# Kernel tuning notes

Measured on AMD Instinct MI355X. Metric: run time of the kernel, lower is better.

Reference implementation:

```python
import jax, jax.numpy as jnp
import numpy as np

TEMP = 1.0

def setup_inputs() -> dict:
    key = jax.random.key(0)
    k1, k2 = jax.random.split(key)
    B, T, C, Vp1 = 16, 2048, 256, 1025
    z = jax.random.normal(k1, (B, T, C), dtype=jnp.float32)
    mask = jnp.ones((B, T, 1), dtype=jnp.float32)
    codebook_weight = jax.random.normal(k2, (Vp1, C), dtype=jnp.float32)
    return {"z": z, "mask": mask, "codebook_weight": codebook_weight}

def reference(z, mask, codebook_weight):
    # e = codebook.embedding.weight.clone().detach()[1:, :]
    e = jax.lax.stop_gradient(codebook_weight[1:, :])  # [V, C]
    b, t, c = z.shape
    V = e.shape[0]
    z_flat = z.reshape(-1, c)                          # [N, C], N = b*t
    # sim(): cosine-sim matmul + log_softmax + argmax one-hot quantize
    cos_sim = jnp.matmul(z_flat, e.T)                  # [N, V]
    log_probs = jax.nn.log_softmax(cos_sim / TEMP, axis=1)
    indices = jnp.argmax(log_probs, axis=1)            # [N]
    # one_hot @ e is exactly a row gather -- avoid materializing one_hot
    z_q = e[indices]                                   # [N, C]
    z_q3 = z_q.reshape(b, t, c)
    # loss(): masked commitment + smoothness
    valid_count = mask.sum() * c
    commitment_loss = (jnp.square(z - jax.lax.stop_gradient(z_q3)) * mask).sum() / valid_count
    smoothness_loss = (jnp.square(z[:, :-1, :] - z[:, 1:, :]) * mask[:, 1:, :]).sum() / valid_count
    # codebook_usage(): (one_hot * mask).sum(0) / mask.sum(), normalized
    mflat = mask.reshape(-1)                           # [N]
    prob = jax.ops.segment_sum(mflat, indices, num_segments=V) / mflat.sum()
    e_mean = prob / prob.sum()
    return (smoothness_loss, commitment_loss, log_probs.reshape(b, t, V), z_q3, e_mean)
```

## Files before the change

kernel.cpp:

```cpp
#include <hip/hip_runtime.h>
#include <hip/hip_bf16.h>

#define TPB 512
#define BM 32
#define NROW 32768
#define NBLK (NROW / BM)
#define VV 1024
#define KD 256
#define TT 2048

#define LP_OFF 2L
#define ZQ_OFF (2L + 33554432L)
#define EM_OFF (33554434L + 8388608L)

#define WS_HIST 0
#define WS_CSUM 1024
#define WS_SSUM 2048
#define WS_MSUM 3072
#define WS_E8 4096
#define WS_Z8G (4096 + 131072)
#define WS_NEED_Z ((size_t)WS_Z8G * 4 + (size_t)NROW * KD * 2)

typedef __attribute__((ext_vector_type(8))) short bf16x8;
typedef __attribute__((ext_vector_type(4))) float f32x4;

__device__ __forceinline__ void gl_lds16(const void* g, void* l) {
  __builtin_amdgcn_global_load_lds(
      (const __attribute__((address_space(1))) void*)g,
      (__attribute__((address_space(3))) void*)l, 16, 0, 0);
}

__device__ __forceinline__ unsigned short f2bf(float x) {
  unsigned u = __float_as_uint(x);
  unsigned r = ((u >> 16) & 1u) + 0x7FFFu;
  return (unsigned short)((u + r) >> 16);
}

__device__ __forceinline__ unsigned foldf(float v) {
  unsigned b = __float_as_uint(v);
  return b ^ ((unsigned)((int)b >> 31) | 0x80000000u);
}
__device__ __forceinline__ float unfoldf(unsigned k) {
  unsigned s = (unsigned)((int)k >> 31);
  return __uint_as_float(k ^ (0x80000000u | (~s & 0x7FFFFFFFu)));
}

__device__ __forceinline__ int4 pack8(const float* p) {
  float4 a = *(const float4*)p;
  float4 b = *(const float4*)(p + 4);
  int4 pk;
  pk.x = f2bf(a.x) | ((unsigned)f2bf(a.y) << 16);
  pk.y = f2bf(a.z) | ((unsigned)f2bf(a.w) << 16);
  pk.z = f2bf(b.x) | ((unsigned)f2bf(b.y) << 16);
  pk.w = f2bf(b.z) | ((unsigned)f2bf(b.w) << 16);
  return pk;
}

__global__ __launch_bounds__(256) void tok_prep(
    const float* __restrict__ z, const float* __restrict__ cw,
    unsigned short* __restrict__ e8, unsigned short* __restrict__ z8g) {
  int t = blockIdx.x * 256 + threadIdx.x;
  if (t < 1048576) {
    int blk = t >> 10, oct = (t >> 5) & 31, row = t & 31;
    *(int4*)(z8g + ((size_t)t << 3)) =
        pack8(z + ((size_t)((blk << 5) + row) << 8) + (oct << 3));
    return;
  }
  int t2 = t - 1048576;
  if (t2 >= 32768) return;
  int s = t2 >> 12, w = (t2 >> 9) & 7, g = (t2 >> 7) & 3, c = t2 & 127;
  int n = (w << 7) + c;
  int o = (s << 2) + g;
  *(int4*)(e8 + ((size_t)t2 << 3)) =
      pack8(cw + ((size_t)(1 + n) << 8) + (o << 3));
}

__global__ __launch_bounds__(TPB, 4) void tok_mfma(
    const float* __restrict__ z, const float* __restrict__ mask,
    const float* __restrict__ cw, const unsigned short* __restrict__ e8,
    const unsigned short* __restrict__ z8g, float* __restrict__ out,
    float* __restrict__ ws) {
  __shared__ __align__(16) unsigned short Bs[32768];
  __shared__ __align__(16) unsigned char apool[4736];
  unsigned(*wkey)[2][33] = (unsigned(*)[2][33])apool;
  float(*wsum)[33] = (float(*)[33])(apool + 2112);
  float* lse_s = (float*)(apool + 3168);
  float(*exv_s)[4] = (float(*)[4])(apool + 3296);
  int(*exi_s)[4] = (int(*)[4])(apool + 3808);
  int* argi = (int*)(apool + 4320);
  float* cred = (float*)(apool + 4448);
  float* sred = (float*)(apool + 4480);

  const int tid = threadIdx.x;
  const int lane = tid & 63;
  const int w = tid >> 6;
  const int g = lane >> 4;
  const int lm = lane & 15;
  const int c0 = w << 7;
  const int n0 = blockIdx.x * BM;

  const bf16x8* Az = (const bf16x8*)z8g + ((size_t)blockIdx.x << 10);

#pragma unroll
  for (int r = 0; r < 8; ++r)
    gl_lds16(e8 + (((w << 9) + (r << 6) + lane) << 3),
             &Bs[(((w << 9) + (r << 6)) + lane) << 3]);

  f32x4 accA[8], accB[8];
  const f32x4 zzero = {0.f, 0.f, 0.f, 0.f};
#pragma unroll
  for (int nt = 0; nt < 8; ++nt) { accA[nt] = zzero; accB[nt] = zzero; }

  bf16x8 a0 = Az[(g << 5) + lm];
  bf16x8 a1 = Az[(g << 5) + 16 + lm];
  const bf16x8* Bl = (const bf16x8*)&Bs[((w << 9) + (g << 7) + lm) << 3];

#pragma unroll 1
  for (int s = 0; s < 8; ++s) {
    asm volatile("s_waitcnt vmcnt(0)" ::: "memory");
    bf16x8 na0, na1;
    if (s < 7) {
      na0 = Az[((((s + 1) << 2) + g) << 5) + lm];
      na1 = Az[((((s + 1) << 2) + g) << 5) + 16 + lm];
    }
#pragma unroll
    for (int nt = 0; nt < 8; ++nt) {
      bf16x8 b = Bl[nt << 4];
      accA[nt] = __builtin_amdgcn_mfma_f32_16x16x32_bf16(a0, b, accA[nt], 0, 0, 0);
      accB[nt] = __builtin_amdgcn_mfma_f32_16x16x32_bf16(a1, b, accB[nt], 0, 0, 0);
    }
    asm volatile("s_waitcnt lgkmcnt(0)" ::: "memory");
    if (s < 7) {
#pragma unroll
      for (int r = 0; r < 8; ++r)
        gl_lds16(e8 + ((((s + 1) << 12) + (w << 9) + (r << 6) + lane) << 3),
                 &Bs[(((w << 9) + (r << 6)) + lane) << 3]);
    }
    a0 = na0;
    a1 = na1;
  }

  unsigned colpack[8];
#pragma unroll
  for (int nt = 0; nt < 8; ++nt)
    colpack[nt] = 1023u - (unsigned)(c0 + (nt << 4) + lm);

  auto phase1 = [&](f32x4(&ac)[8], int mt) {
#pragma unroll
    for (int j = 0; j < 4; ++j) {
      const int r = (mt << 4) + (g << 2) + j;
      unsigned cur[8];
#pragma unroll
      for (int nt = 0; nt < 8; ++nt)
        cur[nt] = (foldf(ac[nt][j]) & 0xFFFFFC00u) | colpack[nt];
      unsigned k1 = cur[0];
#pragma unroll
      for (int nt = 1; nt < 8; ++nt) k1 = k1 > cur[nt] ? k1 : cur[nt];
#pragma unroll
      for (int d = 1; d <= 8; d <<= 1) {
        unsigned o2 = __shfl_xor(k1, d);
        k1 = k1 > o2 ? k1 : o2;
      }
      const float mw = unfoldf(k1 & 0xFFFFFC00u);
      float sum = 0.f;
#pragma unroll
      for (int nt = 0; nt < 8; ++nt) sum += __expf(ac[nt][j] - mw);
#pragma unroll
      for (int d = 1; d <= 8; d <<= 1) sum += __shfl_xor(sum, d);
#pragma unroll
      for (int nt = 0; nt < 8; ++nt)
        if (cur[nt] == k1) cur[nt] = 0u;
      unsigned k2 = cur[0];
#pragma unroll
      for (int nt = 1; nt < 8; ++nt) k2 = k2 > cur[nt] ? k2 : cur[nt];
#pragma unroll
      for (int d = 1; d <= 8; d <<= 1) {
        unsigned o2 = __shfl_xor(k2, d);
        k2 = k2 > o2 ? k2 : o2;
      }
      if (lm == 0) {
        wkey[w][0][r] = k1;
        wkey[w][1][r] = k2;
        wsum[w][r] = sum;
      }
    }
  };
  phase1(accA, 0);
  phase1(accB, 1);
  __syncthreads();

  if (tid < 32) {
    const int r = tid;
    unsigned best[4] = {0u, 0u, 0u, 0u};
#pragma unroll
    for (int w2 = 0; w2 < 8; ++w2)
#pragma unroll
      for (int k = 0; k < 2; ++k) {
        unsigned x = wkey[w2][k][r];
#pragma unroll
        for (int q = 0; q < 4; ++q) {
          unsigned mx = x > best[q] ? x : best[q];
          unsigned mn = x > best[q] ? best[q] : x;
          best[q] = mx;
          x = mn;
        }
      }
    const float M = unfoldf(best[0] & 0xFFFFFC00u);
    float S = 0.f;
#pragma unroll
    for (int w2 = 0; w2 < 8; ++w2)
      S += wsum[w2][r] * __expf(unfoldf(wkey[w2][0][r] & 0xFFFFFC00u) - M);
    lse_s[r] = M + __logf(S);
#pragma unroll
    for (int q = 0; q < 4; ++q) exi_s[r][q] = (int)(1023u - (best[q] & 0x3FFu));
  }
  __syncthreads();

  {
    const int row = (w << 2) + (lane >> 4);
    const int cd = (lane >> 2) & 3;
    const int seg = lane & 3;
    const int cand = exi_s[row][cd];
    const float* er = cw + (size_t)(1 + cand) * KD + (seg << 6);
    const float* zr = z + (size_t)(n0 + row) * KD + (seg << 6);
    float s = 0.f;
#pragma unroll
    for (int i2 = 0; i2 < 16; ++i2) {
      float4 a4 = *(const float4*)(zr + (i2 << 2));
      float4 b4 = *(const float4*)(er + (i2 << 2));
      s += a4.x * b4.x + a4.y * b4.y + a4.z * b4.z + a4.w * b4.w;
    }
    s += __shfl_xor(s, 1);
    s += __shfl_xor(s, 2);
    if (seg == 0) exv_s[row][cd] = s;
  }
  __syncthreads();

  if (tid < 32) {
    const int row = tid;
    float bv = exv_s[row][0];
    int bi = exi_s[row][0];
#pragma unroll
    for (int c = 1; c < 4; ++c) {
      float v = exv_s[row][c];
      int ci = exi_s[row][c];
      if (v > bv || (v == bv && ci < bi)) { bv = v; bi = ci; }
    }
    argi[row] = bi;
    atomicAdd(&ws[WS_HIST + bi], mask[n0 + row]);
  }
  __syncthreads();

  float csum = 0.f, ssum = 0.f;
  float4 evs[4];
  const bool has_prev = (n0 % TT) != 0;
#pragma unroll
  for (int i = 0; i < 4; ++i) {
    const int r = (i << 3) + w;
    const int c4 = lane << 2;
    const int idx = argi[r];
    const float4 ev = *(const float4*)&cw[(size_t)(1 + idx) * KD + c4];
    evs[i] = ev;
    const float4 zv = *(const float4*)&z[(size_t)(n0 + r) * KD + c4];
    const float mk = mask[n0 + r];
    float dx = zv.x - ev.x, dy = zv.y - ev.y, dz2 = zv.z - ev.z,
          dw = zv.w - ev.w;
    csum += mk * (dx * dx + dy * dy + dz2 * dz2 + dw * dw);
    if (r > 0 || has_prev) {
      const float4 pv = *(const float4*)&z[(size_t)(n0 + r - 1) * KD + c4];
      float ax = zv.x - pv.x, ay = zv.y - pv.y, az = zv.z - pv.z,
            aw = zv.w - pv.w;
      ssum += mk * (ax * ax + ay * ay + az * az + aw * aw);
    }
  }
#pragma unroll
  for (int d = 1; d <= 32; d <<= 1) {
    csum += __shfl_xor(csum, d);
    ssum += __shfl_xor(ssum, d);
  }
  if (lane == 0) { cred[w] = csum; sred[w] = ssum; }
  __syncthreads();
  if (tid == 0) {
    float cs = 0.f, ss2 = 0.f;
#pragma unroll
    for (int i = 0; i < 8; ++i) { cs += cred[i]; ss2 += sred[i]; }
    ws[WS_CSUM + blockIdx.x] = cs;
    ws[WS_SSUM + blockIdx.x] = ss2;
    float ms = 0.f;
    for (int r2 = 0; r2 < BM; ++r2) ms += mask[n0 + r2];
    ws[WS_MSUM + blockIdx.x] = ms;
  }

#pragma unroll
  for (int i = 0; i < 4; ++i) {
    const int r = (i << 3) + w;
    *(float4*)&out[ZQ_OFF + (size_t)(n0 + r) * KD + (lane << 2)] = evs[i];
  }
  auto phase3 = [&](f32x4(&ac)[8], int mt) {
#pragma unroll
    for (int j = 0; j < 4; ++j) {
      const int r = (mt << 4) + (g << 2) + j;
      const float lse = lse_s[r];
      size_t base = LP_OFF + (size_t)(n0 + r) * VV;
#pragma unroll
      for (int nt = 0; nt < 8; ++nt)
        out[base + c0 + (nt << 4) + lm] = ac[nt][j] - lse;
    }
  };
  phase3(accA, 0);
  phase3(accB, 1);
}

__global__ __launch_bounds__(256, 2) void tok_fb(
    const float* __restrict__ z, const float* __restrict__ mask,
    const float* __restrict__ cw, float* __restrict__ out,
    float* __restrict__ ws) {
  __shared__ __align__(16) float z_s[BM][KD];
  __shared__ int argi_s[BM];
  __shared__ float cred[4], sred[4];
  const int tid = threadIdx.x;
  const int lane = tid & 63;
  const int wave = tid >> 6;
  const int n0 = blockIdx.x * BM;
  const float* e = cw + KD;
#pragma unroll
  for (int i = 0; i < 8; ++i) {
    int seg = wave * 8 + i;
    gl_lds16(&z[(size_t)(n0 + seg) * KD + lane * 4], &z_s[seg][0]);
  }
  __syncthreads();
  float acc[8][16];
#pragma unroll
  for (int r = 0; r < 8; ++r)
#pragma unroll
    for (int m = 0; m < 16; ++m) acc[r][m] = 0.f;
#pragma unroll 1
  for (int i = 0; i < 64; ++i) {
    float4 ef[16];
#pragma unroll
    for (int m = 0; m < 16; ++m)
      ef[m] = *(const float4*)&e[(size_t)((m << 6) + lane) * KD + (i << 2)];
    float4 zf[8];
#pragma unroll
    for (int rr = 0; rr < 8; ++rr)
      zf[rr] = *(const float4*)&z_s[(wave << 3) + rr][i << 2];
#pragma unroll
    for (int m = 0; m < 16; ++m)
#pragma unroll
      for (int rr = 0; rr < 8; ++rr)
        acc[rr][m] += zf[rr].x * ef[m].x + zf[rr].y * ef[m].y +
                      zf[rr].z * ef[m].z + zf[rr].w * ef[m].w;
  }
  const int rowbase = wave << 3;
#pragma unroll
  for (int rr = 0; rr < 8; ++rr) {
    float mv = acc[rr][0];
    int mc = lane;
#pragma unroll
    for (int m = 1; m < 16; ++m) {
      float v = acc[rr][m];
      int c = (m << 6) + lane;
      bool tk = v > mv;
      mc = tk ? c : mc;
      mv = tk ? v : mv;
    }
#pragma unroll
    for (int d = 32; d >= 1; d >>= 1) {
      float ov = __shfl_xor(mv, d);
      int oc = __shfl_xor(mc, d);
      bool tk = (ov > mv) || (ov == mv && oc < mc);
      mv = tk ? ov : mv;
      mc = tk ? oc : mc;
    }
    float sum = 0.f;
#pragma unroll
    for (int m = 0; m < 16; ++m) sum += __expf(acc[rr][m] - mv);
#pragma unroll
    for (int d = 32; d >= 1; d >>= 1) sum += __shfl_xor(sum, d);
    float lse = mv + __logf(sum);
    size_t base = LP_OFF + (size_t)(n0 + rowbase + rr) * VV;
#pragma unroll
    for (int m = 0; m < 16; ++m) out[base + (m << 6) + lane] = acc[rr][m] - lse;
    if (lane == 0) {
      argi_s[rowbase + rr] = mc;
      atomicAdd(&ws[WS_HIST + mc], mask[n0 + rowbase + rr]);
    }
  }
  __syncthreads();
  float csum = 0.f, ssum = 0.f;
  const bool has_prev = (n0 % TT) != 0;
#pragma unroll
  for (int i = 0; i < 8; ++i) {
    int q = i * 256 + tid;
    int r = q >> 6;
    int c4 = (q & 63) << 2;
    int idx = argi_s[r];
    const float4 ev = *(const float4*)&e[(size_t)idx * KD + c4];
    const float4 zv = *(const float4*)&z_s[r][c4];
    *(float4*)&out[ZQ_OFF + (size_t)(n0 + r) * KD + c4] = ev;
    float mk = mask[n0 + r];
    float dx = zv.x - ev.x, dy = zv.y - ev.y, dz2 = zv.z - ev.z, dw = zv.w - ev.w;
    csum += mk * (dx * dx + dy * dy + dz2 * dz2 + dw * dw);
    if (r > 0) {
      const float4 pv = *(const float4*)&z_s[r - 1][c4];
      float ax = zv.x - pv.x, ay = zv.y - pv.y, az = zv.z - pv.z, aw = zv.w - pv.w;
      ssum += mk * (ax * ax + ay * ay + az * az + aw * aw);
    } else if (has_prev) {
      const float4 pv = *(const float4*)&z[(size_t)(n0 - 1) * KD + c4];
      float ax = zv.x - pv.x, ay = zv.y - pv.y, az = zv.z - pv.z, aw = zv.w - pv.w;
      ssum += mk * (ax * ax + ay * ay + az * az + aw * aw);
    }
  }
#pragma unroll
  for (int d = 32; d >= 1; d >>= 1) {
    csum += __shfl_xor(csum, d);
    ssum += __shfl_xor(ssum, d);
  }
  if (lane == 0) { cred[wave] = csum; sred[wave] = ssum; }
  __syncthreads();
  if (tid == 0) {
    ws[WS_CSUM + blockIdx.x] = cred[0] + cred[1] + cred[2] + cred[3];
    ws[WS_SSUM + blockIdx.x] = sred[0] + sred[1] + sred[2] + sred[3];
    float ms = 0.f;
    for (int r2 = 0; r2 < BM; ++r2) ms += mask[n0 + r2];
    ws[WS_MSUM + blockIdx.x] = ms;
  }
}

__global__ __launch_bounds__(1024) void tok_final(const float* __restrict__ ws,
                                                  float* __restrict__ out) {
  const int t = threadIdx.x;
  const int lane = t & 63, w = t >> 6;
  __shared__ float red[16];
  auto blockReduce = [&](float v) -> float {
#pragma unroll
    for (int d = 32; d >= 1; d >>= 1) v += __shfl_xor(v, d);
    __syncthreads();
    if (lane == 0) red[w] = v;
    __syncthreads();
    float s = 0.f;
#pragma unroll
    for (int i = 0; i < 16; ++i) s += red[i];
    return s;
  };
  float Mtot = blockReduce(ws[WS_MSUM + t]);
  float Ctot = blockReduce(ws[WS_CSUM + t]);
  float Stot = blockReduce(ws[WS_SSUM + t]);
  float prob = ws[WS_HIST + t] / Mtot;
  float psum = blockReduce(prob);
  out[EM_OFF + t] = prob / psum;
  if (t == 0) {
    float vc = Mtot * (float)KD;
    out[0] = Stot / vc;
    out[1] = Ctot / vc;
  }
}

extern "C" void kernel_launch(void* const* d_in, const int* in_sizes, int n_in,
                              void* d_out, int out_size, void* d_ws,
                              size_t ws_size, hipStream_t stream) {
  const float* z = (const float*)d_in[0];
  const float* mask = (const float*)d_in[1];
  const float* cw = (const float*)d_in[2];
  float* out = (float*)d_out;
  float* ws = (float*)d_ws;
  hipMemsetAsync(ws, 0, 1024 * sizeof(float), stream);
  if (ws_size >= WS_NEED_Z) {
    unsigned short* e8 = (unsigned short*)(ws + WS_E8);
    unsigned short* z8g = (unsigned short*)(ws + WS_Z8G);
    tok_prep<<<4224, 256, 0, stream>>>(z, cw, e8, z8g);
    tok_mfma<<<NBLK, TPB, 0, stream>>>(z, mask, cw, e8, z8g, out, ws);
  } else {
    tok_fb<<<NBLK, 256, 0, stream>>>(z, mask, cw, out, ws);
  }
  tok_final<<<1, 1024, 0, stream>>>(ws, out);
}
```

Baseline: 117.8 us.

## Enlarge row tile to 64 with 16 waves and double-buffered codebook staging

Each block now covers 64 rows with 1024 threads (16 waves), so every wave owns 64 codebook columns. Z tiles are staged into LDS instead of being read per wave from global memory. Codebook slices are loaded as two half-buffers so the global-to-LDS copy of one half overlaps MFMA work on the other. This halves the block count and per-row B traffic, and mask reads now go through LDS. In exchange it uses more LDS per block and more threads per block, which may limit occupancy.

```diff
diff --git a/kernel.cpp b/kernel.cpp
--- a/kernel.cpp
+++ b/kernel.cpp
@@ -1,10 +1,9 @@
 #include <hip/hip_runtime.h>
 #include <hip/hip_bf16.h>
 
-#define TPB 512
-#define BM 32
+#define BM 64
 #define NROW 32768
-#define NBLK (NROW / BM)
+#define NB2 (NROW / BM)
 #define VV 1024
 #define KD 256
 #define TT 2048
@@ -61,101 +60,125 @@
     unsigned short* __restrict__ e8, unsigned short* __restrict__ z8g) {
   int t = blockIdx.x * 256 + threadIdx.x;
   if (t < 1048576) {
-    int blk = t >> 10, oct = (t >> 5) & 31, row = t & 31;
+    int blk = t >> 11, oct = (t >> 6) & 31, row = t & 63;
     *(int4*)(z8g + ((size_t)t << 3)) =
-        pack8(z + ((size_t)((blk << 5) + row) << 8) + (oct << 3));
+        pack8(z + (size_t)((blk << 6) + row) * KD + (oct << 3));
     return;
   }
   int t2 = t - 1048576;
   if (t2 >= 32768) return;
-  int s = t2 >> 12, w = (t2 >> 9) & 7, g = (t2 >> 7) & 3, c = t2 & 127;
-  int n = (w << 7) + c;
-  int o = (s << 2) + g;
-  *(int4*)(e8 + ((size_t)t2 << 3)) =
-      pack8(cw + ((size_t)(1 + n) << 8) + (o << 3));
-}
-
-__global__ __launch_bounds__(TPB, 4) void tok_mfma(
+  int s = t2 >> 12, w2 = (t2 >> 8) & 15, h = (t2 >> 7) & 1,
+      qq = (t2 >> 6) & 1, gp = (t2 >> 5) & 1, c = t2 & 31;
+  int n = (w2 << 6) + (h << 5) + c;
+  int o = (s << 2) + (qq << 1) + gp;
+  *(int4*)(e8 + ((size_t)t2 << 3)) = pack8(cw + (size_t)(1 + n) * KD + (o << 3));
+}
+
+__global__ __launch_bounds__(1024, 4) void tok_mfma(
     const float* __restrict__ z, const float* __restrict__ mask,
     const float* __restrict__ cw, const unsigned short* __restrict__ e8,
     const unsigned short* __restrict__ z8g, float* __restrict__ out,
     float* __restrict__ ws) {
-  __shared__ __align__(16) unsigned short Bs[32768];
-  __shared__ __align__(16) unsigned char apool[4736];
-  unsigned(*wkey)[2][33] = (unsigned(*)[2][33])apool;
-  float(*wsum)[33] = (float(*)[33])(apool + 2112);
-  float* lse_s = (float*)(apool + 3168);
-  float(*exv_s)[4] = (float(*)[4])(apool + 3296);
-  int(*exi_s)[4] = (int(*)[4])(apool + 3808);
-  int* argi = (int*)(apool + 4320);
-  float* cred = (float*)(apool + 4448);
-  float* sred = (float*)(apool + 4480);
+  __shared__ __align__(16) unsigned short A_s[16640];
+  __shared__ __align__(16) unsigned short B_s[32768];
+  __shared__ unsigned wkey[16][2][65];
+  __shared__ float wsum[16][65];
+  __shared__ float lse_s[64];
+  __shared__ float exv_s[64][4];
+  __shared__ int exi_s[64][4];
+  __shared__ int argi[64];
+  __shared__ float mask_s[64];
+  __shared__ float cred[16], sred[16];
 
   const int tid = threadIdx.x;
   const int lane = tid & 63;
   const int w = tid >> 6;
   const int g = lane >> 4;
   const int lm = lane & 15;
-  const int c0 = w << 7;
-  const int n0 = blockIdx.x * BM;
-
-  const bf16x8* Az = (const bf16x8*)z8g + ((size_t)blockIdx.x << 10);
-
-#pragma unroll
-  for (int r = 0; r < 8; ++r)
-    gl_lds16(e8 + (((w << 9) + (r << 6) + lane) << 3),
-             &Bs[(((w << 9) + (r << 6)) + lane) << 3]);
-
-  f32x4 accA[8], accB[8];
+  const int q = g >> 1, g2 = g & 1;
+  const int n0 = blockIdx.x << 6;
+
+  unsigned short* Bw = B_s + (w << 11);
+
+  {
+    const unsigned short* asrc =
+        z8g + ((((size_t)blockIdx.x << 11) + (w << 7)) << 3) + (lane << 3);
+    gl_lds16(asrc, A_s + (w << 1) * 520);
+    gl_lds16(asrc + 512, A_s + ((w << 1) + 1) * 520);
+  }
+  if (tid < 64) mask_s[tid] = mask[n0 + tid];
+  __syncthreads();
+
+  auto stage_half = [&](int s2, int h2, int bufb) {
+    const unsigned short* src =
+        e8 + ((size_t)((((s2 << 4) + w) << 2) + (h2 << 1)) << 9) + (lane << 3);
+    unsigned short* dst = Bw + (bufb << 10);
+    gl_lds16(src, dst);
+    gl_lds16(src + 512, dst + 512);
+  };
+  stage_half(0, 0, 0);
+  stage_half(0, 1, 1);
+
+  f32x4 acc[4][4];
   const f32x4 zzero = {0.f, 0.f, 0.f, 0.f};
 #pragma unroll
-  for (int nt = 0; nt < 8; ++nt) { accA[nt] = zzero; accB[nt] = zzero; }
-
-  bf16x8 a0 = Az[(g << 5) + lm];
-  bf16x8 a1 = Az[(g << 5) + 16 + lm];
-  const bf16x8* Bl = (const bf16x8*)&Bs[((w << 9) + (g << 7) + lm) << 3];
+  for (int mt = 0; mt < 4; ++mt)
+#pragma unroll
+    for (int nt = 0; nt < 4; ++nt) acc[mt][nt] = zzero;
+
+  const int boff = (q << 9) + (g2 << 8) + (lm << 3);
 
 #pragma unroll 1
   for (int s = 0; s < 8; ++s) {
-    asm volatile("s_waitcnt vmcnt(0)" ::: "memory");
-    bf16x8 na0, na1;
-    if (s < 7) {
-      na0 = Az[((((s + 1) << 2) + g) << 5) + lm];
-      na1 = Az[((((s + 1) << 2) + g) << 5) + 16 + lm];
-    }
-#pragma unroll
-    for (int nt = 0; nt < 8; ++nt) {
-      bf16x8 b = Bl[nt << 4];
-      accA[nt] = __builtin_amdgcn_mfma_f32_16x16x32_bf16(a0, b, accA[nt], 0, 0, 0);
-      accB[nt] = __builtin_amdgcn_mfma_f32_16x16x32_bf16(a1, b, accB[nt], 0, 0, 0);
+    asm volatile("s_waitcnt vmcnt(2)" ::: "memory");
+    bf16x8 a[4];
+#pragma unroll
+    for (int mt = 0; mt < 4; ++mt)
+      a[mt] = *(const bf16x8*)(A_s + ((s << 2) + g) * 520 +
+                               (((mt << 4) + lm) << 3));
+#pragma unroll
+    for (int l = 0; l < 2; ++l) {
+      bf16x8 b = *(const bf16x8*)(Bw + boff + (l << 7));
+#pragma unroll
+      for (int mt = 0; mt < 4; ++mt)
+        acc[mt][l] =
+            __builtin_amdgcn_mfma_f32_16x16x32_bf16(a[mt], b, acc[mt][l], 0, 0, 0);
     }
     asm volatile("s_waitcnt lgkmcnt(0)" ::: "memory");
-    if (s < 7) {
-#pragma unroll
-      for (int r = 0; r < 8; ++r)
-        gl_lds16(e8 + ((((s + 1) << 12) + (w << 9) + (r << 6) + lane) << 3),
-                 &Bs[(((w << 9) + (r << 6)) + lane) << 3]);
-    }
-    a0 = na0;
-    a1 = na1;
-  }
-
-  unsigned colpack[8];
-#pragma unroll
-  for (int nt = 0; nt < 8; ++nt)
-    colpack[nt] = 1023u - (unsigned)(c0 + (nt << 4) + lm);
-
-  auto phase1 = [&](f32x4(&ac)[8], int mt) {
+    if (s < 7) stage_half(s + 1, 0, 0);
+    if (s < 7)
+      asm volatile("s_waitcnt vmcnt(2)" ::: "memory");
+    else
+      asm volatile("s_waitcnt vmcnt(0)" ::: "memory");
+#pragma unroll
+    for (int l = 0; l < 2; ++l) {
+      bf16x8 b = *(const bf16x8*)(Bw + 1024 + boff + (l << 7));
+#pragma unroll
+      for (int mt = 0; mt < 4; ++mt)
+        acc[mt][2 + l] = __builtin_amdgcn_mfma_f32_16x16x32_bf16(
+            a[mt], b, acc[mt][2 + l], 0, 0, 0);
+    }
+    asm volatile("s_waitcnt lgkmcnt(0)" ::: "memory");
+    if (s < 7) stage_half(s + 1, 1, 1);
+  }
+
+  unsigned colpack[4];
+#pragma unroll
+  for (int nt = 0; nt < 4; ++nt)
+    colpack[nt] = 1023u - (unsigned)((w << 6) + (nt << 4) + lm);
+
+#pragma unroll
+  for (int mt = 0; mt < 4; ++mt)
 #pragma unroll
     for (int j = 0; j < 4; ++j) {
       const int r = (mt << 4) + (g << 2) + j;
-      unsigned cur[8];
-#pragma unroll
-      for (int nt = 0; nt < 8; ++nt)
-        cur[nt] = (foldf(ac[nt][j]) & 0xFFFFFC00u) | colpack[nt];
+      unsigned cur[4];
+#pragma unroll
+      for (int nt = 0; nt < 4; ++nt)
+        cur[nt] = (foldf(acc[mt][nt][j]) & 0xFFFFFC00u) | colpack[nt];
       unsigned k1 = cur[0];
 #pragma unroll
-      for (int nt = 1; nt < 8; ++nt) k1 = k1 > cur[nt] ? k1 : cur[nt];
+      for (int nt = 1; nt < 4; ++nt) k1 = k1 > cur[nt] ? k1 : cur[nt];
 #pragma unroll
       for (int d = 1; d <= 8; d <<= 1) {
         unsigned o2 = __shfl_xor(k1, d);
@@ -164,15 +187,15 @@
       const float mw = unfoldf(k1 & 0xFFFFFC00u);
       float sum = 0.f;
 #pragma unroll
-      for (int nt = 0; nt < 8; ++nt) sum += __expf(ac[nt][j] - mw);
+      for (int nt = 0; nt < 4; ++nt) sum += __expf(acc[mt][nt][j] - mw);
 #pragma unroll
       for (int d = 1; d <= 8; d <<= 1) sum += __shfl_xor(sum, d);
 #pragma unroll
-      for (int nt = 0; nt < 8; ++nt)
+      for (int nt = 0; nt < 4; ++nt)
         if (cur[nt] == k1) cur[nt] = 0u;
       unsigned k2 = cur[0];
 #pragma unroll
-      for (int nt = 1; nt < 8; ++nt) k2 = k2 > cur[nt] ? k2 : cur[nt];
+      for (int nt = 1; nt < 4; ++nt) k2 = k2 > cur[nt] ? k2 : cur[nt];
 #pragma unroll
       for (int d = 1; d <= 8; d <<= 1) {
         unsigned o2 = __shfl_xor(k2, d);
@@ -184,42 +207,40 @@
         wsum[w][r] = sum;
       }
     }
-  };
-  phase1(accA, 0);
-  phase1(accB, 1);
-  __syncthreads();
-
-  if (tid < 32) {
+  __syncthreads();
+
+  if (tid < 64) {
     const int r = tid;
     unsigned best[4] = {0u, 0u, 0u, 0u};
 #pragma unroll
-    for (int w2 = 0; w2 < 8; ++w2)
+    for (int w2 = 0; w2 < 16; ++w2)
 #pragma unroll
       for (int k = 0; k < 2; ++k) {
         unsigned x = wkey[w2][k][r];
 #pragma unroll
-        for (int q = 0; q < 4; ++q) {
-          unsigned mx = x > best[q] ? x : best[q];
-          unsigned mn = x > best[q] ? best[q] : x;
-          best[q] = mx;
+        for (int p2 = 0; p2 < 4; ++p2) {
+          unsigned mx = x > best[p2] ? x : best[p2];
+          unsigned mn = x > best[p2] ? best[p2] : x;
+          best[p2] = mx;
           x = mn;
         }
       }
     const float M = unfoldf(best[0] & 0xFFFFFC00u);
     float S = 0.f;
 #pragma unroll
-    for (int w2 = 0; w2 < 8; ++w2)
+    for (int w2 = 0; w2 < 16; ++w2)
       S += wsum[w2][r] * __expf(unfoldf(wkey[w2][0][r] & 0xFFFFFC00u) - M);
     lse_s[r] = M + __logf(S);
 #pragma unroll
-    for (int q = 0; q < 4; ++q) exi_s[r][q] = (int)(1023u - (best[q] & 0x3FFu));
+    for (int p2 = 0; p2 < 4; ++p2)
+      exi_s[r][p2] = (int)(1023u - (best[p2] & 0x3FFu));
   }
   __syncthreads();
 
   {
-    const int row = (w << 2) + (lane >> 4);
-    const int cd = (lane >> 2) & 3;
-    const int seg = lane & 3;
+    const int row = tid >> 4;
+    const int cd = (tid >> 2) & 3;
+    const int seg = tid & 3;
     const int cand = exi_s[row][cd];
     const float* er = cw + (size_t)(1 + cand) * KD + (seg << 6);
     const float* zr = z + (size_t)(n0 + row) * KD + (seg << 6);
@@ -236,7 +257,7 @@
   }
   __syncthreads();
 
-  if (tid < 32) {
+  if (tid < 64) {
     const int row = tid;
     float bv = exv_s[row][0];
     int bi = exi_s[row][0];
@@ -247,7 +268,7 @@
       if (v > bv || (v == bv && ci < bi)) { bv = v; bi = ci; }
     }
     argi[row] = bi;
-    atomicAdd(&ws[WS_HIST + bi], mask[n0 + row]);
+    atomicAdd(&ws[WS_HIST + bi], mask_s[row]);
   }
   __syncthreads();
 
@@ -256,13 +277,13 @@
   const bool has_prev = (n0 % TT) != 0;
 #pragma unroll
   for (int i = 0; i < 4; ++i) {
-    const int r = (i << 3) + w;
+    const int r = (i << 4) + w;
     const int c4 = lane << 2;
     const int idx = argi[r];
     const float4 ev = *(const float4*)&cw[(size_t)(1 + idx) * KD + c4];
     evs[i] = ev;
     const float4 zv = *(const float4*)&z[(size_t)(n0 + r) * KD + c4];
-    const float mk = mask[n0 + r];
+    const float mk = mask_s[r];
     float dx = zv.x - ev.x, dy = zv.y - ev.y, dz2 = zv.z - ev.z,
           dw = zv.w - ev.w;
     csum += mk * (dx * dx + dy * dy + dz2 * dz2 + dw * dw);
@@ -283,45 +304,43 @@
   if (tid == 0) {
     float cs = 0.f, ss2 = 0.f;
 #pragma unroll
-    for (int i = 0; i < 8; ++i) { cs += cred[i]; ss2 += sred[i]; }
+    for (int i = 0; i < 16; ++i) { cs += cred[i]; ss2 += sred[i]; }
     ws[WS_CSUM + blockIdx.x] = cs;
     ws[WS_SSUM + blockIdx.x] = ss2;
     float ms = 0.f;
-    for (int r2 = 0; r2 < BM; ++r2) ms += mask[n0 + r2];
+    for (int r2 = 0; r2 < 64; ++r2) ms += mask_s[r2];
     ws[WS_MSUM + blockIdx.x] = ms;
   }
 
 #pragma unroll
   for (int i = 0; i < 4; ++i) {
-    const int r = (i << 3) + w;
+    const int r = (i << 4) + w;
     *(float4*)&out[ZQ_OFF + (size_t)(n0 + r) * KD + (lane << 2)] = evs[i];
   }
-  auto phase3 = [&](f32x4(&ac)[8], int mt) {
+#pragma unroll
+  for (int mt = 0; mt < 4; ++mt)
 #pragma unroll
     for (int j = 0; j < 4; ++j) {
       const int r = (mt << 4) + (g << 2) + j;
       const float lse = lse_s[r];
-      size_t base = LP_OFF + (size_t)(n0 + r) * VV;
-#pragma unroll
-      for (int nt = 0; nt < 8; ++nt)
-        out[base + c0 + (nt << 4) + lm] = ac[nt][j] - lse;
-    }
-  };
-  phase3(accA, 0);
-  phase3(accB, 1);
+      size_t base = LP_OFF + (size_t)(n0 + r) * VV + (w << 6);
+#pragma unroll
+      for (int nt = 0; nt < 4; ++nt)
+        out[base + (nt << 4) + lm] = acc[mt][nt][j] - lse;
+    }
 }
 
 __global__ __launch_bounds__(256, 2) void tok_fb(
     const float* __restrict__ z, const float* __restrict__ mask,
     const float* __restrict__ cw, float* __restrict__ out,
     float* __restrict__ ws) {
-  __shared__ __align__(16) float z_s[BM][KD];
-  __shared__ int argi_s[BM];
+  __shared__ __align__(16) float z_s[32][KD];
+  __shared__ int argi_s[32];
   __shared__ float cred[4], sred[4];
   const int tid = threadIdx.x;
   const int lane = tid & 63;
   const int wave = tid >> 6;
-  const int n0 = blockIdx.x * BM;
+  const int n0 = blockIdx.x * 32;
   const float* e = cw + KD;
 #pragma unroll
   for (int i = 0; i < 8; ++i) {
@@ -422,11 +441,12 @@
     ws[WS_CSUM + blockIdx.x] = cred[0] + cred[1] + cred[2] + cred[3];
     ws[WS_SSUM + blockIdx.x] = sred[0] + sred[1] + sred[2] + sred[3];
     float ms = 0.f;
-    for (int r2 = 0; r2 < BM; ++r2) ms += mask[n0 + r2];
+    for (int r2 = 0; r2 < 32; ++r2) ms += mask[n0 + r2];
     ws[WS_MSUM + blockIdx.x] = ms;
   }
 }
 
+template <int NB>
 __global__ __launch_bounds__(1024) void tok_final(const float* __restrict__ ws,
                                                   float* __restrict__ out) {
   const int t = threadIdx.x;
@@ -443,9 +463,9 @@
     for (int i = 0; i < 16; ++i) s += red[i];
     return s;
   };
-  float Mtot = blockReduce(ws[WS_MSUM + t]);
-  float Ctot = blockReduce(ws[WS_CSUM + t]);
-  float Stot = blockReduce(ws[WS_SSUM + t]);
+  float Mtot = blockReduce(t < NB ? ws[WS_MSUM + t] : 0.f);
+  float Ctot = blockReduce(t < NB ? ws[WS_CSUM + t] : 0.f);
+  float Stot = blockReduce(t < NB ? ws[WS_SSUM + t] : 0.f);
   float prob = ws[WS_HIST + t] / Mtot;
   float psum = blockReduce(prob);
   out[EM_OFF + t] = prob / psum;
@@ -469,9 +489,10 @@
     unsigned short* e8 = (unsigned short*)(ws + WS_E8);
     unsigned short* z8g = (unsigned short*)(ws + WS_Z8G);
     tok_prep<<<4224, 256, 0, stream>>>(z, cw, e8, z8g);
-    tok_mfma<<<NBLK, TPB, 0, stream>>>(z, mask, cw, e8, z8g, out, ws);
+    tok_mfma<<<NB2, 1024, 0, stream>>>(z, mask, cw, e8, z8g, out, ws);
+    tok_final<NB2><<<1, 1024, 0, stream>>>(ws, out);
   } else {
-    tok_fb<<<NBLK, 256, 0, stream>>>(z, mask, cw, out, ws);
-  }
-  tok_final<<<1, 1024, 0, stream>>>(ws, out);
-}
+    tok_fb<<<NROW / 32, 256, 0, stream>>>(z, mask, cw, out, ws);
+    tok_final<NROW / 32><<<1, 1024, 0, stream>>>(ws, out);
+  }
+}
```

Measured after the change: 123.0 us. +4.4%, slower.

## Convert z to bf16 in-kernel via swizzled LDS and stream codebook from global

Applied to the files above, without the earlier changes.

Drops the prep pass that converted all of z to bf16 in workspace. Each block now packs its own 32 rows of z into a swizzled LDS tile, and codebook fragments are read directly from global (L2) into registers with a double-buffered software pipeline instead of being staged through a 64KB LDS buffer. The LDS footprint shrinks, which may raise occupancy. Logits and z_q outputs are written with nontemporal stores to limit cache pollution. The risk is that B fragments read from global may stall the MFMAs more than the LDS path did.

```diff
diff --git a/kernel.cpp b/kernel.cpp
--- a/kernel.cpp
+++ b/kernel.cpp
@@ -18,8 +18,7 @@
 #define WS_SSUM 2048
 #define WS_MSUM 3072
 #define WS_E8 4096
-#define WS_Z8G (4096 + 131072)
-#define WS_NEED_Z ((size_t)WS_Z8G * 4 + (size_t)NROW * KD * 2)
+#define WS_NEED ((size_t)(4096 + 131072) * 4)
 
 typedef __attribute__((ext_vector_type(8))) short bf16x8;
 typedef __attribute__((ext_vector_type(4))) float f32x4;
@@ -56,40 +55,28 @@
   return pk;
 }
 
-__global__ __launch_bounds__(256) void tok_prep(
-    const float* __restrict__ z, const float* __restrict__ cw,
-    unsigned short* __restrict__ e8, unsigned short* __restrict__ z8g) {
+__global__ __launch_bounds__(256) void tok_prep(const float* __restrict__ cw,
+                                                unsigned short* __restrict__ e8) {
   int t = blockIdx.x * 256 + threadIdx.x;
-  if (t < 1048576) {
-    int blk = t >> 10, oct = (t >> 5) & 31, row = t & 31;
-    *(int4*)(z8g + ((size_t)t << 3)) =
-        pack8(z + ((size_t)((blk << 5) + row) << 8) + (oct << 3));
-    return;
-  }
-  int t2 = t - 1048576;
-  if (t2 >= 32768) return;
-  int s = t2 >> 12, w = (t2 >> 9) & 7, g = (t2 >> 7) & 3, c = t2 & 127;
+  int s = t >> 12, w = (t >> 9) & 7, g = (t >> 7) & 3, c = t & 127;
   int n = (w << 7) + c;
   int o = (s << 2) + g;
-  *(int4*)(e8 + ((size_t)t2 << 3)) =
-      pack8(cw + ((size_t)(1 + n) << 8) + (o << 3));
+  *(int4*)(e8 + ((size_t)t << 3)) = pack8(cw + (size_t)(1 + n) * KD + (o << 3));
 }
 
 __global__ __launch_bounds__(TPB, 4) void tok_mfma(
     const float* __restrict__ z, const float* __restrict__ mask,
     const float* __restrict__ cw, const unsigned short* __restrict__ e8,
-    const unsigned short* __restrict__ z8g, float* __restrict__ out,
-    float* __restrict__ ws) {
-  __shared__ __align__(16) unsigned short Bs[32768];
-  __shared__ __align__(16) unsigned char apool[4736];
-  unsigned(*wkey)[2][33] = (unsigned(*)[2][33])apool;
-  float(*wsum)[33] = (float(*)[33])(apool + 2112);
-  float* lse_s = (float*)(apool + 3168);
-  float(*exv_s)[4] = (float(*)[4])(apool + 3296);
-  int(*exi_s)[4] = (int(*)[4])(apool + 3808);
-  int* argi = (int*)(apool + 4320);
-  float* cred = (float*)(apool + 4448);
-  float* sred = (float*)(apool + 4480);
+    float* __restrict__ out, float* __restrict__ ws) {
+  __shared__ __align__(16) unsigned char smem[16384];
+  unsigned(*wkey)[2][33] = (unsigned(*)[2][33])smem;
+  float(*wsum)[33] = (float(*)[33])(smem + 2112);
+  float* lse_s = (float*)(smem + 3168);
+  float(*exv_s)[4] = (float(*)[4])(smem + 3296);
+  int(*exi_s)[4] = (int(*)[4])(smem + 3808);
+  int* argi = (int*)(smem + 4320);
+  float* cred = (float*)(smem + 4448);
+  float* sred = (float*)(smem + 4480);
 
   const int tid = threadIdx.x;
   const int lane = tid & 63;
@@ -99,46 +86,62 @@
   const int c0 = w << 7;
   const int n0 = blockIdx.x * BM;
 
-  const bf16x8* Az = (const bf16x8*)z8g + ((size_t)blockIdx.x << 10);
-
-#pragma unroll
-  for (int r = 0; r < 8; ++r)
-    gl_lds16(e8 + (((w << 9) + (r << 6) + lane) << 3),
-             &Bs[(((w << 9) + (r << 6)) + lane) << 3]);
-
+  {
+    const int zr = (w << 2) + (lane >> 4);
+    const int oc0 = lm << 1;
+    const float* zp = z + (size_t)(n0 + zr) * KD + (lm << 4);
+    int4 p0 = pack8(zp);
+    int4 p1 = pack8(zp + 8);
+    const int i0 = (oc0 << 5) + (zr ^ ((oc0 & 7) << 2));
+    const int i1 = ((oc0 + 1) << 5) + (zr ^ (((oc0 + 1) & 7) << 2));
+    *(int4*)&smem[i0 << 4] = p0;
+    *(int4*)&smem[i1 << 4] = p1;
+  }
+  __syncthreads();
+
+  const bf16x8* Bp = (const bf16x8*)e8 + ((w << 9) + (g << 7) + lm);
   f32x4 accA[8], accB[8];
   const f32x4 zzero = {0.f, 0.f, 0.f, 0.f};
 #pragma unroll
   for (int nt = 0; nt < 8; ++nt) { accA[nt] = zzero; accB[nt] = zzero; }
 
-  bf16x8 a0 = Az[(g << 5) + lm];
-  bf16x8 a1 = Az[(g << 5) + 16 + lm];
-  const bf16x8* Bl = (const bf16x8*)&Bs[((w << 9) + (g << 7) + lm) << 3];
-
-#pragma unroll 1
-  for (int s = 0; s < 8; ++s) {
-    asm volatile("s_waitcnt vmcnt(0)" ::: "memory");
-    bf16x8 na0, na1;
-    if (s < 7) {
-      na0 = Az[((((s + 1) << 2) + g) << 5) + lm];
-      na1 = Az[((((s + 1) << 2) + g) << 5) + 16 + lm];
-    }
-#pragma unroll
-    for (int nt = 0; nt < 8; ++nt) {
-      bf16x8 b = Bl[nt << 4];
-      accA[nt] = __builtin_amdgcn_mfma_f32_16x16x32_bf16(a0, b, accA[nt], 0, 0, 0);
-      accB[nt] = __builtin_amdgcn_mfma_f32_16x16x32_bf16(a1, b, accB[nt], 0, 0, 0);
-    }
-    asm volatile("s_waitcnt lgkmcnt(0)" ::: "memory");
-    if (s < 7) {
-#pragma unroll
-      for (int r = 0; r < 8; ++r)
-        gl_lds16(e8 + ((((s + 1) << 12) + (w << 9) + (r << 6) + lane) << 3),
-                 &Bs[(((w << 9) + (r << 6)) + lane) << 3]);
-    }
-    a0 = na0;
-    a1 = na1;
-  }
+  bf16x8 q0, q1, q2, q3, q4, q5, q6, q7;
+  bf16x8 r0, r1, r2, r3, r4, r5, r6, r7;
+#define LOAD8(P, T)                                                      \
+  P##0 = Bp[((T) << 12)];        P##1 = Bp[((T) << 12) + 16];            \
+  P##2 = Bp[((T) << 12) + 32];   P##3 = Bp[((T) << 12) + 48];            \
+  P##4 = Bp[((T) << 12) + 64];   P##5 = Bp[((T) << 12) + 80];            \
+  P##6 = Bp[((T) << 12) + 96];   P##7 = Bp[((T) << 12) + 112];           \
+  __builtin_amdgcn_sched_barrier(0);
+#define MFMA1(A0, A1, BV, NT)                                            \
+  accA[NT] = __builtin_amdgcn_mfma_f32_16x16x32_bf16(A0, BV, accA[NT], 0, 0, 0); \
+  accB[NT] = __builtin_amdgcn_mfma_f32_16x16x32_bf16(A1, BV, accB[NT], 0, 0, 0);
+#define STEP(P, T)                                                       \
+  {                                                                      \
+    const int oct = ((T) << 2) + g;                                      \
+    const int swz = (oct & 7) << 2;                                      \
+    bf16x8 a0 = *(const bf16x8*)&smem[((oct << 5) + (lm ^ swz)) << 4];   \
+    bf16x8 a1 =                                                          \
+        *(const bf16x8*)&smem[((oct << 5) + ((16 + lm) ^ swz)) << 4];    \
+    MFMA1(a0, a1, P##0, 0) MFMA1(a0, a1, P##1, 1) MFMA1(a0, a1, P##2, 2) \
+    MFMA1(a0, a1, P##3, 3) MFMA1(a0, a1, P##4, 4) MFMA1(a0, a1, P##5, 5) \
+    MFMA1(a0, a1, P##6, 6) MFMA1(a0, a1, P##7, 7)                        \
+  }
+  LOAD8(q, 0)
+  LOAD8(r, 1)
+  STEP(q, 0) LOAD8(q, 2)
+  STEP(r, 1) LOAD8(r, 3)
+  STEP(q, 2) LOAD8(q, 4)
+  STEP(r, 3) LOAD8(r, 5)
+  STEP(q, 4) LOAD8(q, 6)
+  STEP(r, 5) LOAD8(r, 7)
+  STEP(q, 6)
+  STEP(r, 7)
+#undef STEP
+#undef MFMA1
+#undef LOAD8
+
+  __syncthreads();
 
   unsigned colpack[8];
 #pragma unroll
@@ -252,24 +255,24 @@
   __syncthreads();
 
   float csum = 0.f, ssum = 0.f;
-  float4 evs[4];
+  f32x4 evs[4];
   const bool has_prev = (n0 % TT) != 0;
 #pragma unroll
   for (int i = 0; i < 4; ++i) {
     const int r = (i << 3) + w;
     const int c4 = lane << 2;
     const int idx = argi[r];
-    const float4 ev = *(const float4*)&cw[(size_t)(1 + idx) * KD + c4];
+    const f32x4 ev = *(const f32x4*)&cw[(size_t)(1 + idx) * KD + c4];
     evs[i] = ev;
-    const float4 zv = *(const float4*)&z[(size_t)(n0 + r) * KD + c4];
+    const f32x4 zv = *(const f32x4*)&z[(size_t)(n0 + r) * KD + c4];
     const float mk = mask[n0 + r];
-    float dx = zv.x - ev.x, dy = zv.y - ev.y, dz2 = zv.z - ev.z,
-          dw = zv.w - ev.w;
+    float dx = zv[0] - ev[0], dy = zv[1] - ev[1], dz2 = zv[2] - ev[2],
+          dw = zv[3] - ev[3];
     csum += mk * (dx * dx + dy * dy + dz2 * dz2 + dw * dw);
     if (r > 0 || has_prev) {
-      const float4 pv = *(const float4*)&z[(size_t)(n0 + r - 1) * KD + c4];
-      float ax = zv.x - pv.x, ay = zv.y - pv.y, az = zv.z - pv.z,
-            aw = zv.w - pv.w;
+      const f32x4 pv = *(const f32x4*)&z[(size_t)(n0 + r - 1) * KD + c4];
+      float ax = zv[0] - pv[0], ay = zv[1] - pv[1], az = zv[2] - pv[2],
+            aw = zv[3] - pv[3];
       ssum += mk * (ax * ax + ay * ay + az * az + aw * aw);
     }
   }
@@ -294,7 +297,8 @@
 #pragma unroll
   for (int i = 0; i < 4; ++i) {
     const int r = (i << 3) + w;
-    *(float4*)&out[ZQ_OFF + (size_t)(n0 + r) * KD + (lane << 2)] = evs[i];
+    __builtin_nontemporal_store(
+        evs[i], (f32x4*)&out[ZQ_OFF + (size_t)(n0 + r) * KD + (lane << 2)]);
   }
   auto phase3 = [&](f32x4(&ac)[8], int mt) {
 #pragma unroll
@@ -304,7 +308,8 @@
       size_t base = LP_OFF + (size_t)(n0 + r) * VV;
 #pragma unroll
       for (int nt = 0; nt < 8; ++nt)
-        out[base + c0 + (nt << 4) + lm] = ac[nt][j] - lse;
+        __builtin_nontemporal_store(ac[nt][j] - lse,
+                                    &out[base + c0 + (nt << 4) + lm]);
     }
   };
   phase3(accA, 0);
@@ -464,12 +469,11 @@
   const float* cw = (const float*)d_in[2];
   float* out = (float*)d_out;
   float* ws = (float*)d_ws;
-  hipMemsetAsync(ws, 0, 1024 * sizeof(float), stream);
-  if (ws_size >= WS_NEED_Z) {
+  (void)hipMemsetAsync(ws, 0, 1024 * sizeof(float), stream);
+  if (ws_size >= WS_NEED) {
     unsigned short* e8 = (unsigned short*)(ws + WS_E8);
-    unsigned short* z8g = (unsigned short*)(ws + WS_Z8G);
-    tok_prep<<<4224, 256, 0, stream>>>(z, cw, e8, z8g);
-    tok_mfma<<<NBLK, TPB, 0, stream>>>(z, mask, cw, e8, z8g, out, ws);
+    tok_prep<<<128, 256, 0, stream>>>(cw, e8);
+    tok_mfma<<<NBLK, TPB, 0, stream>>>(z, mask, cw, e8, out, ws);
   } else {
     tok_fb<<<NBLK, 256, 0, stream>>>(z, mask, cw, out, ws);
   }
```

Measured after the change: 198.8 us. 68.7% more time.
